# Kernel optimization log

Hardware: AMD Instinct MI355X
Metric: run time of the kernel (lower is better)

## Reference

```python
import jax, jax.numpy as jnp
import numpy as np

LN_EPS = 1e-7

def gelu(x):
    # BERT erf-based gelu
    return 0.5 * x * (1.0 + jax.lax.erf(x / jnp.sqrt(2.0).astype(x.dtype)))

def setup_inputs() -> dict:
    key = jax.random.key(0)
    k1, k2 = jax.random.split(key)
    B, S, H, I = 4, 4096, 1024, 4096
    hidden_states = jax.random.normal(k1, (B, S, H), dtype=jnp.float32)
    W = jax.random.normal(k2, (H, I), dtype=jnp.float32) * (1.0 / np.sqrt(H))
    b = jnp.zeros((I,), dtype=jnp.float32)
    ln_gamma = jnp.ones((H,), dtype=jnp.float32)
    ln_beta = jnp.zeros((H,), dtype=jnp.float32)
    return {"hidden_states": hidden_states, "ln_gamma": ln_gamma, "ln_beta": ln_beta, "W": W, "b": b}

def reference(hidden_states, ln_gamma, ln_beta, W, b):
    # LayerNorm over last dim
    mu = jnp.mean(hidden_states, axis=-1, keepdims=True)
    xc = hidden_states - mu
    var = jnp.mean(xc * xc, axis=-1, keepdims=True)
    x_norm = xc * jax.lax.rsqrt(var + LN_EPS) * ln_gamma + ln_beta
    # Linear projection [B,S,H] @ [H,I] + b, then gelu
    y = jnp.einsum('bsh,hi->bsi', x_norm, W) + b
    return gelu(y)
```

## Files before the change

kernel.cpp:

```cpp
#include <hip/hip_runtime.h>
#include <hip/hip_bf16.h>

typedef __attribute__((ext_vector_type(8))) short bf16x8;
typedef __attribute__((ext_vector_type(4))) float f32x4;

static __device__ __forceinline__ unsigned short f2bf(float f) {
    unsigned u = __builtin_bit_cast(unsigned, f);
    unsigned rounding = 0x7fffu + ((u >> 16) & 1u);
    u += rounding;
    return (unsigned short)(u >> 16);
}

static __device__ __forceinline__ void async_copy16(const void* g, void* l) {
    __builtin_amdgcn_global_load_lds(
        (const __attribute__((address_space(1))) unsigned int*)g,
        (__attribute__((address_space(3))) unsigned int*)l,
        16, 0, 0);
}

#define BARRIER() __builtin_amdgcn_s_barrier()
#define LGKM0()  do { asm volatile("s_waitcnt lgkmcnt(0)" ::: "memory"); \
                      __builtin_amdgcn_sched_barrier(0); } while (0)
#define VM0()    do { asm volatile("s_waitcnt vmcnt(0)" ::: "memory"); \
                      __builtin_amdgcn_sched_barrier(0); } while (0)

static __device__ __forceinline__ float fast_gelu(float y) {
    float u = 0.7978845608028654f * y * (1.0f + 0.044715f * y * y);
    float au = fminf(fabsf(u), 9.0f);
    float e = __expf(-2.0f * au);
    float th = (1.0f - e) * __builtin_amdgcn_rcpf(1.0f + e);
    th = (u < 0.0f) ? -th : th;
    return 0.5f * y * (1.0f + th);
}

__global__ __launch_bounds__(256) void ln_cast_kernel(
    const float* __restrict__ x, const float* __restrict__ gamma,
    const float* __restrict__ beta, unsigned short* __restrict__ out) {
    const int row = blockIdx.x;
    const int t = threadIdx.x;
    const float4 v = ((const float4*)(x + (size_t)row * 1024))[t];

    float s  = v.x + v.y + v.z + v.w;
    float ss = v.x * v.x + v.y * v.y + v.z * v.z + v.w * v.w;
    #pragma unroll
    for (int off = 32; off; off >>= 1) {
        s  += __shfl_down(s, off);
        ss += __shfl_down(ss, off);
    }
    __shared__ float red[8];
    const int wid = t >> 6, lane = t & 63;
    if (lane == 0) { red[wid] = s; red[wid + 4] = ss; }
    __syncthreads();
    if (t == 0) {
        float S  = red[0] + red[1] + red[2] + red[3];
        float SS = red[4] + red[5] + red[6] + red[7];
        float mu = S * (1.0f / 1024.0f);
        float var = SS * (1.0f / 1024.0f) - mu * mu;
        red[0] = mu;
        red[1] = rsqrtf(var + 1e-7f);
    }
    __syncthreads();
    const float mu = red[0], rs = red[1];
    const float4 g = ((const float4*)gamma)[t];
    const float4 b = ((const float4*)beta)[t];

    ushort4 pk;
    pk.x = f2bf((v.x - mu) * rs * g.x + b.x);
    pk.y = f2bf((v.y - mu) * rs * g.y + b.y);
    pk.z = f2bf((v.z - mu) * rs * g.z + b.z);
    pk.w = f2bf((v.w - mu) * rs * g.w + b.w);
    ((ushort4*)(out + (size_t)row * 1024))[t] = pk;
}

__global__ __launch_bounds__(256) void wt_cast_kernel(
    const float* __restrict__ W, unsigned short* __restrict__ Wt) {
    __shared__ float tile[32][33];
    const int bx = blockIdx.x;
    const int by = blockIdx.y;
    const int tx = threadIdx.x & 31;
    const int ty = threadIdx.x >> 5;
    #pragma unroll
    for (int i = 0; i < 4; ++i) {
        int k = by * 32 + ty + i * 8;
        tile[ty + i * 8][tx] = W[(size_t)k * 4096 + bx * 32 + tx];
    }
    __syncthreads();
    #pragma unroll
    for (int i = 0; i < 4; ++i) {
        int n = bx * 32 + ty + i * 8;
        Wt[(size_t)n * 1024 + by * 32 + tx] = f2bf(tile[tx][ty + i * 8]);
    }
}

__global__ __launch_bounds__(256, 2) void gemm_kernel(
    const unsigned short* __restrict__ A, const unsigned short* __restrict__ Wt,
    const float* __restrict__ bias, float* __restrict__ out) {
    __shared__ char lds_mem[65536];

    const int bid = blockIdx.x;
    const int swz = (bid & 7) * 512 + (bid >> 3);
    const int bm = swz >> 5;
    const int bn = swz & 31;

    const int t = threadIdx.x;
    const int lane = t & 63;
    const int wid = t >> 6;
    const int wm = wid >> 1, wn = wid & 1;
    const int lrow = lane & 15;
    const int lk = lane >> 4;

    const int srr = t >> 3;
    const int sch = t & 7;
    const int sgc = sch ^ (srr & 7);
    const unsigned short* gA = A  + (size_t)(bm * 128 + srr) * 1024 + sgc * 8;
    const unsigned short* gB = Wt + (size_t)(bn * 128 + srr) * 1024 + sgc * 8;
    const int lst = srr * 128 + sch * 16;

    auto stage = [&](int kt, char* buf) {
        #pragma unroll
        for (int i = 0; i < 4; ++i) {
            async_copy16(gA + (size_t)(i * 32) * 1024 + kt * 64, buf + i * 32 * 128 + lst);
            async_copy16(gB + (size_t)(i * 32) * 1024 + kt * 64, buf + 16384 + i * 32 * 128 + lst);
        }
    };

    const int ck0 = ((lk) ^ (lrow & 7)) * 16;
    const int ck1 = ((4 + lk) ^ (lrow & 7)) * 16;
    const int aBase = (wm * 64 + lrow) * 128;
    const int bBase = 16384 + (wn * 64 + lrow) * 128;

    f32x4 acc[4][4];
    #pragma unroll
    for (int i = 0; i < 4; ++i)
        #pragma unroll
        for (int j = 0; j < 4; ++j) acc[i][j] = (f32x4)0.0f;

    stage(0, lds_mem);
    VM0();
    BARRIER();

    const int NKT = 16;
    for (int kt = 0; kt < NKT; ++kt) {
        char* cbuf = lds_mem + ((kt & 1) << 15);
        char* nbuf = lds_mem + (((kt + 1) & 1) << 15);

        if (kt + 1 < NKT) stage(kt + 1, nbuf);

        bf16x8 af[4][2], bf[4][2];
        #pragma unroll
        for (int mi = 0; mi < 4; ++mi) {
            const char* p = cbuf + aBase + mi * 16 * 128;
            af[mi][0] = *(const bf16x8*)(p + ck0);
            af[mi][1] = *(const bf16x8*)(p + ck1);
        }
        #pragma unroll
        for (int ni = 0; ni < 4; ++ni) {
            const char* p = cbuf + bBase + ni * 16 * 128;
            bf[ni][0] = *(const bf16x8*)(p + ck0);
            bf[ni][1] = *(const bf16x8*)(p + ck1);
        }
        LGKM0();
        __builtin_amdgcn_s_setprio(1);
        #pragma unroll
        for (int mi = 0; mi < 4; ++mi)
            #pragma unroll
            for (int ni = 0; ni < 4; ++ni) {
                acc[mi][ni] = __builtin_amdgcn_mfma_f32_16x16x32_bf16(af[mi][0], bf[ni][0], acc[mi][ni], 0, 0, 0);
                acc[mi][ni] = __builtin_amdgcn_mfma_f32_16x16x32_bf16(af[mi][1], bf[ni][1], acc[mi][ni], 0, 0, 0);
            }
        __builtin_amdgcn_s_setprio(0);
        VM0();
        BARRIER();
    }

    float bv[4];
    #pragma unroll
    for (int ni = 0; ni < 4; ++ni) bv[ni] = bias[bn * 128 + wn * 64 + ni * 16 + lrow];
    #pragma unroll
    for (int mi = 0; mi < 4; ++mi) {
        const int row0 = bm * 128 + wm * 64 + mi * 16 + lk * 4;
        #pragma unroll
        for (int ni = 0; ni < 4; ++ni) {
            const int col = bn * 128 + wn * 64 + ni * 16 + lrow;
            #pragma unroll
            for (int r = 0; r < 4; ++r) {
                float y = acc[mi][ni][r] + bv[ni];
                out[(size_t)(row0 + r) * 4096 + col] = fast_gelu(y);
            }
        }
    }
}

extern "C" void kernel_launch(void* const* d_in, const int* in_sizes, int n_in,
                              void* d_out, int out_size, void* d_ws, size_t ws_size,
                              hipStream_t stream) {
    const float* hidden = (const float*)d_in[0];
    const float* gamma  = (const float*)d_in[1];
    const float* beta   = (const float*)d_in[2];
    const float* W      = (const float*)d_in[3];
    const float* bias   = (const float*)d_in[4];
    float* out = (float*)d_out;

    unsigned short* Abf = (unsigned short*)d_ws;
    unsigned short* Wt  = (unsigned short*)((char*)d_ws + (size_t)16384 * 1024 * 2);

    ln_cast_kernel<<<16384, 256, 0, stream>>>(hidden, gamma, beta, Abf);
    wt_cast_kernel<<<dim3(128, 32), 256, 0, stream>>>(W, Wt);
    gemm_kernel<<<4096, 256, 0, stream>>>(Abf, Wt, bias, out);
}
```

Baseline: 207.1 us.

## Switch GEMM to triple-buffered K=32 stages with partial vmcnt waits

The GEMM main loop moves from double-buffered K=64 tiles to three 16KB K=32 buffers, prefetching two stages ahead and waiting with vmcnt(4) instead of draining all loads every iteration. The smaller LDS footprint (48KB) allows launch bounds of 3 blocks per CU for higher occupancy. The LDS swizzle is reworked for the 64-byte row pitch. The trade-off is twice as many iterations and barriers with half the MFMA work between each, plus more register pressure at the higher occupancy target.

```diff
diff --git a/kernel.cpp b/kernel.cpp
--- a/kernel.cpp
+++ b/kernel.cpp
@@ -20,8 +20,6 @@
 
 #define BARRIER() __builtin_amdgcn_s_barrier()
 #define LGKM0()  do { asm volatile("s_waitcnt lgkmcnt(0)" ::: "memory"); \
-                      __builtin_amdgcn_sched_barrier(0); } while (0)
-#define VM0()    do { asm volatile("s_waitcnt vmcnt(0)" ::: "memory"); \
                       __builtin_amdgcn_sched_barrier(0); } while (0)
 
 static __device__ __forceinline__ float fast_gelu(float y) {
@@ -92,10 +90,10 @@
     }
 }
 
-__global__ __launch_bounds__(256, 2) void gemm_kernel(
+__global__ __launch_bounds__(256, 3) void gemm_kernel(
     const unsigned short* __restrict__ A, const unsigned short* __restrict__ Wt,
     const float* __restrict__ bias, float* __restrict__ out) {
-    __shared__ char lds_mem[65536];
+    __shared__ char lds_mem[49152];
 
     const int bid = blockIdx.x;
     const int swz = (bid & 7) * 512 + (bid >> 3);
@@ -109,68 +107,71 @@
     const int lrow = lane & 15;
     const int lk = lane >> 4;
 
-    const int srr = t >> 3;
-    const int sch = t & 7;
-    const int sgc = sch ^ (srr & 7);
-    const unsigned short* gA = A  + (size_t)(bm * 128 + srr) * 1024 + sgc * 8;
-    const unsigned short* gB = Wt + (size_t)(bn * 128 + srr) * 1024 + sgc * 8;
-    const int lst = srr * 128 + sch * 16;
+    const int srow = t >> 2;
+    const int sc = (t & 3) ^ ((t >> 3) & 3);
+    const unsigned short* gA0 = A  + (size_t)(bm * 128 + srow) * 1024 + sc * 8;
+    const unsigned short* gB0 = Wt + (size_t)(bn * 128 + srow) * 1024 + sc * 8;
+    const int lslot = t * 16;
 
     auto stage = [&](int kt, char* buf) {
-        #pragma unroll
-        for (int i = 0; i < 4; ++i) {
-            async_copy16(gA + (size_t)(i * 32) * 1024 + kt * 64, buf + i * 32 * 128 + lst);
-            async_copy16(gB + (size_t)(i * 32) * 1024 + kt * 64, buf + 16384 + i * 32 * 128 + lst);
+        async_copy16(gA0 + kt * 32,                    buf + lslot);
+        async_copy16(gA0 + (size_t)64 * 1024 + kt * 32, buf + 4096 + lslot);
+        async_copy16(gB0 + kt * 32,                    buf + 8192 + lslot);
+        async_copy16(gB0 + (size_t)64 * 1024 + kt * 32, buf + 12288 + lslot);
+    };
+
+    const int swzc = (lk ^ ((lrow >> 1) & 3)) * 16;
+    const int aOff = (wm * 64 + lrow) * 64 + swzc;
+    const int bOff = 8192 + (wn * 64 + lrow) * 64 + swzc;
+
+    f32x4 acc[4][4];
+    #pragma unroll
+    for (int i = 0; i < 4; ++i)
+        #pragma unroll
+        for (int j = 0; j < 4; ++j) acc[i][j] = (f32x4)0.0f;
+
+    stage(0, lds_mem);
+    stage(1, lds_mem + 16384);
+    asm volatile("s_waitcnt vmcnt(4)" ::: "memory");
+    __builtin_amdgcn_sched_barrier(0);
+    BARRIER();
+
+    const int NKT = 32;
+    int cb = 0;
+    for (int kt = 0; kt < NKT; ++kt) {
+        char* cbuf = lds_mem + cb * 16384;
+        if (kt + 2 < NKT) {
+            char* sbuf = lds_mem + ((cb >= 1) ? (cb - 1) : 2) * 16384;
+            stage(kt + 2, sbuf);
         }
-    };
-
-    const int ck0 = ((lk) ^ (lrow & 7)) * 16;
-    const int ck1 = ((4 + lk) ^ (lrow & 7)) * 16;
-    const int aBase = (wm * 64 + lrow) * 128;
-    const int bBase = 16384 + (wn * 64 + lrow) * 128;
-
-    f32x4 acc[4][4];
-    #pragma unroll
-    for (int i = 0; i < 4; ++i)
-        #pragma unroll
-        for (int j = 0; j < 4; ++j) acc[i][j] = (f32x4)0.0f;
-
-    stage(0, lds_mem);
-    VM0();
-    BARRIER();
-
-    const int NKT = 16;
-    for (int kt = 0; kt < NKT; ++kt) {
-        char* cbuf = lds_mem + ((kt & 1) << 15);
-        char* nbuf = lds_mem + (((kt + 1) & 1) << 15);
-
-        if (kt + 1 < NKT) stage(kt + 1, nbuf);
-
-        bf16x8 af[4][2], bf[4][2];
-        #pragma unroll
-        for (int mi = 0; mi < 4; ++mi) {
-            const char* p = cbuf + aBase + mi * 16 * 128;
-            af[mi][0] = *(const bf16x8*)(p + ck0);
-            af[mi][1] = *(const bf16x8*)(p + ck1);
-        }
-        #pragma unroll
-        for (int ni = 0; ni < 4; ++ni) {
-            const char* p = cbuf + bBase + ni * 16 * 128;
-            bf[ni][0] = *(const bf16x8*)(p + ck0);
-            bf[ni][1] = *(const bf16x8*)(p + ck1);
-        }
+
+        bf16x8 af[4], bf[4];
+        #pragma unroll
+        for (int mi = 0; mi < 4; ++mi)
+            af[mi] = *(const bf16x8*)(cbuf + aOff + mi * 16 * 64);
+        #pragma unroll
+        for (int ni = 0; ni < 4; ++ni)
+            bf[ni] = *(const bf16x8*)(cbuf + bOff + ni * 16 * 64);
         LGKM0();
         __builtin_amdgcn_s_setprio(1);
         #pragma unroll
         for (int mi = 0; mi < 4; ++mi)
             #pragma unroll
-            for (int ni = 0; ni < 4; ++ni) {
-                acc[mi][ni] = __builtin_amdgcn_mfma_f32_16x16x32_bf16(af[mi][0], bf[ni][0], acc[mi][ni], 0, 0, 0);
-                acc[mi][ni] = __builtin_amdgcn_mfma_f32_16x16x32_bf16(af[mi][1], bf[ni][1], acc[mi][ni], 0, 0, 0);
-            }
+            for (int ni = 0; ni < 4; ++ni)
+                acc[mi][ni] = __builtin_amdgcn_mfma_f32_16x16x32_bf16(
+                    af[mi], bf[ni], acc[mi][ni], 0, 0, 0);
         __builtin_amdgcn_s_setprio(0);
-        VM0();
-        BARRIER();
+
+        if (kt <= NKT - 3) {
+            asm volatile("s_waitcnt vmcnt(4)" ::: "memory");
+            __builtin_amdgcn_sched_barrier(0);
+            BARRIER();
+        } else if (kt == NKT - 2) {
+            asm volatile("s_waitcnt vmcnt(0)" ::: "memory");
+            __builtin_amdgcn_sched_barrier(0);
+            BARRIER();
+        }
+        cb = (cb == 2) ? 0 : cb + 1;
     }
 
     float bv[4];
```

Result: slower. 235.6 us (+13.8%).
